# Performance work log

Hardware: AMD Instinct MI355X
Metric: run time of the kernel (lower is better)

## Reference

```python
import jax, jax.numpy as jnp
import numpy as np

N = 16384; C = 16; H = 256; W = 704
HEADS = 4; PTS = 4; K = 8; DH = C // HEADS
EPS = 1e-3  # BatchNorm eps from module

def _bn(x, g, b):
    # BatchNorm1d in training mode: batch statistics over N
    mu = x.mean(axis=0)
    var = x.var(axis=0)
    return (x - mu) * jax.lax.rsqrt(var + EPS) * g + b

def setup_inputs():
    key = jax.random.key(0)
    ks = jax.random.split(key, 20)
    def w(i, shape, s=0.25):
        return jax.random.normal(ks[i], shape, jnp.float32) * s
    grid_y = jax.random.randint(ks[0], (N,), 0, H)
    grid_x = jax.random.randint(ks[1], (N,), 0, W)
    return {
        "point_features": jax.random.normal(ks[2], (N, C), jnp.float32),
        "image_feat": jax.random.normal(ks[3], (C, H, W), jnp.float32),
        "image_grid": jnp.stack([grid_y, grid_x], axis=1),
        "Wk": w(4, (C, C)), "bk": w(5, (C,)), "gk": jnp.ones((C,)), "betak": jnp.zeros((C,)),
        "Wfc": w(6, (2, C)), "bfc": w(7, (C,)), "gfc": jnp.ones((C,)), "betafc": jnp.zeros((C,)),
        "Wt": w(8, (C, C)), "bt": w(9, (C,)), "gt": jnp.ones((C,)), "betat": jnp.zeros((C,)),
        "Woff": w(10, (C, HEADS * PTS * 2), 0.02), "boff": w(11, (HEADS * PTS * 2,), 0.5),
        "Wattn": w(12, (C, HEADS * PTS), 0.02), "battn": jnp.zeros((HEADS * PTS,)),
        "Wval": w(13, (C, C)), "bval": w(14, (C,)),
        "Wout": w(15, (C, C)), "bout": w(16, (C,)),
        "Wf": w(17, (2 * C, C)), "bf": w(18, (C,)), "gf": jnp.ones((C,)), "betaf": jnp.zeros((C,)),
    }

def _deform_attn(q, image_feat, grid_f, Woff, boff, Wattn, battn, Wval, bval, Wout, bout):
    # MSDeformAttn with 1 level: learned offsets around projected pixel, bilinear sampling
    n = q.shape[0]
    off = (q @ Woff + boff).reshape(n, HEADS, PTS, 2)
    attn = jax.nn.softmax((q @ Wattn + battn).reshape(n, HEADS, PTS), axis=-1)
    val = (image_feat.reshape(C, H * W).T @ Wval + bval).reshape(H * W, HEADS, DH)
    val_h = val.transpose(1, 0, 2)  # [HEADS, HW, DH]
    loc_y = grid_f[:, 0][:, None, None] + off[..., 0]  # [N, HEADS, PTS]
    loc_x = grid_f[:, 1][:, None, None] + off[..., 1]
    y0 = jnp.floor(loc_y); x0 = jnp.floor(loc_x)
    wy = loc_y - y0; wx = loc_x - x0

    def corner(yi, xi, wgt):
        valid = (yi >= 0) & (yi <= H - 1) & (xi >= 0) & (xi <= W - 1)
        yc = jnp.clip(yi, 0, H - 1).astype(jnp.int32)
        xc = jnp.clip(xi, 0, W - 1).astype(jnp.int32)
        idx = (yc * W + xc).transpose(1, 0, 2)  # [HEADS, N, PTS]
        g = jax.vmap(lambda v, i: v[i])(val_h, idx)  # [HEADS, N, PTS, DH]
        return g * (wgt * valid).transpose(1, 0, 2)[..., None]

    samp = (corner(y0, x0, (1 - wy) * (1 - wx))
            + corner(y0, x0 + 1, (1 - wy) * wx)
            + corner(y0 + 1, x0, wy * (1 - wx))
            + corner(y0 + 1, x0 + 1, wy * wx))  # [HEADS, N, PTS, DH]
    out = (samp * attn.transpose(1, 0, 2)[..., None]).sum(axis=2)  # [HEADS, N, DH]
    out = out.transpose(1, 0, 2).reshape(n, C)
    return out @ Wout + bout

def reference(point_features, image_feat, image_grid, Wk, bk, gk, betak, Wfc, bfc, gfc, betafc, Wt, bt, gt, betat, Woff, boff, Wattn, battn, Wval, bval, Wout, bout, Wf, bf, gf, betaf):
    grid_f = image_grid.astype(jnp.float32)
    # KNN over projected pixel coords (cKDTree.query k=K+1, drop self)
    d2 = ((grid_f[:, None, :] - grid_f[None, :, :]) ** 2).sum(-1)
    _, nidx = jax.lax.top_k(-d2, K + 1)
    nidx = nidx[:, 1:]  # [N, K]

    pts = _bn(point_features @ Wk + bk, gk, betak)  # pts_key_proj
    # normalized relative image-plane positions -> fc
    center = grid_f.mean(axis=0)
    rel = grid_f - center
    mx = jnp.abs(rel).max(axis=0)
    mx = jnp.where(mx == 0, 1.0, mx)
    pos = _bn((rel / mx) @ Wfc + bfc, gfc, betafc)

    # gather image feats at projected pixels + KNN-graph neighbor aggregation
    gathered = image_feat[:, image_grid[:, 0], image_grid[:, 1]].T  # [N, C]
    neigh = gathered[nidx].mean(axis=1)  # [N, C]

    q = pts + pos
    img_pre = _deform_attn(q, image_feat, grid_f, Woff, boff, Wattn, battn, Wval, bval, Wout, bout) + neigh

    pts_pre = _bn(pts @ Wt + bt, gt, betat)  # pts_transform
    fuse = jax.nn.relu(jnp.concatenate([pts_pre, img_pre], axis=-1))  # activate_out
    return jax.nn.relu(_bn(fuse @ Wf + bf, gf, betaf))  # fuse_conv
```

## Files before the change

### kernel.cpp

```cpp
#include <hip/hip_runtime.h>
#include <climits>

#define N_ 16384
#define H_ 256
#define W_ 704
#define HW_ (H_*W_)
#define NC_ (N_*16)
#define EPS_ 1e-3f
#define HDR_ 512

typedef unsigned long long ull;

#define VAL_   (HDR_ + 9*NC_)
#define KNNI_  (VAL_ + HW_*16)
#define PARTF_ (KNNI_ + 378256)
#define PK_    (PARTF_ + 8192)
#define PFC_   (PARTF_ + 16384)
#define PT_    (PARTF_ + 24576)

#define CAP_ 6144

__device__ __forceinline__ float wsum64(float v){
#pragma unroll
  for (int o = 32; o > 0; o >>= 1) v += __shfl_down(v, o);
  return v;
}

#define LOAD16(dst, src) { const float4* _s=(const float4*)(src); float4 _a=_s[0],_b=_s[1],_c=_s[2],_d=_s[3]; \
  dst[0]=_a.x;dst[1]=_a.y;dst[2]=_a.z;dst[3]=_a.w; dst[4]=_b.x;dst[5]=_b.y;dst[6]=_b.z;dst[7]=_b.w; \
  dst[8]=_c.x;dst[9]=_c.y;dst[10]=_c.z;dst[11]=_c.w; dst[12]=_d.x;dst[13]=_d.y;dst[14]=_d.z;dst[15]=_d.w; }

#define STORE16(dst, src) { float4* _d=(float4*)(dst); \
  _d[0]=make_float4(src[0],src[1],src[2],src[3]); _d[1]=make_float4(src[4],src[5],src[6],src[7]); \
  _d[2]=make_float4(src[8],src[9],src[10],src[11]); _d[3]=make_float4(src[12],src[13],src[14],src[15]); }

__device__ __forceinline__ void knn_insert(ull* arr, ull key){
  if (key < arr[8]){
    int q = 8;
    while (q > 0 && arr[q-1] > key){ arr[q] = arr[q-1]; --q; }
    arr[q] = key;
  }
}

__device__ __forceinline__ void scan_rows_global(const int* __restrict__ cellst,
                                                 const unsigned* __restrict__ psort,
                                                 int y, int x, int s,
                                                 int y0, int y1, int x0, int x1, ull* arr){
  for (int yy=y0+s; yy<=y1; yy+=4){
    int rowb = yy*W_;
    int st = cellst[rowb + x0];
    int e  = cellst[rowb + x1 + 1];
    int dy = y-yy, dy2 = dy*dy;
    for (int p=st; p<e; ++p){
      unsigned u = psort[p];
      int px = (int)((u>>14)&1023);
      int dx = x-px;
      knn_insert(arr, ((ull)(unsigned)(dy2+dx*dx) << 14) | (ull)(u & 16383u));
    }
  }
}

__device__ __forceinline__ void red_body(const float* __restrict__ g, const float* __restrict__ bta,
                                         const float* __restrict__ part, float* __restrict__ coef,
                                         float* __restrict__ red){
  int t = threadIdx.x, slot = t & 31, chunk = t >> 5;
  float acc = 0.f;
  for (int bb=chunk*32; bb<chunk*32+32; ++bb) acc += part[bb*32 + slot];
  red[t] = acc;
  __syncthreads();
  if (chunk == 0){
    float v = red[slot];
#pragma unroll
    for (int k2=1;k2<8;++k2) v += red[k2*32+slot];
    red[slot] = v;
  }
  __syncthreads();
  if (t < 16){
    float mu  = red[t]    * (1.f/N_);
    float var = red[16+t] * (1.f/N_) - mu*mu;
    float a = g[t] / sqrtf(var + EPS_);
    coef[t]    = a;
    coef[16+t] = bta[t] - mu*a;
  }
  __syncthreads();
}

__global__ __launch_bounds__(256) void k1(const float* __restrict__ pf,
                                          const float* __restrict__ imf,
                                          const int* __restrict__ grid,
                                          const float* __restrict__ Wk, const float* __restrict__ bk,
                                          const float* __restrict__ Wval, const float* __restrict__ bval,
                                          float* __restrict__ ws){
  __shared__ float sA[256], sB[16];
  const int t = threadIdx.x, b = blockIdx.x;
  const bool ldsK = (b >= 177 && b < 241);
  const bool ldsV = (b >= 1265);
  if (ldsK){ sA[t] = Wk[t];   if (t < 16) sB[t] = bk[t]; }
  if (ldsV){ sA[t] = Wval[t]; if (t < 16) sB[t] = bval[t]; }
  if (ldsK || ldsV) __syncthreads();

  if (b < 176){
    int4* c4 = (int4*)(ws + KNNI_);
    c4[b*256 + t] = make_int4(0,0,0,0);
  } else if (b == 176){
    if (t == 0){
      int* ih = (int*)ws;
      ih[0]=0; ih[1]=0; ih[2]=INT_MAX; ih[3]=INT_MIN; ih[4]=INT_MAX; ih[5]=INT_MIN;
      ih[6]=0; ih[7]=0;
    }
  } else if (ldsK){
    const int i = (b-177)*256 + t;
    float p[16]; LOAD16(p, pf + i*16);
    float ok[16];
#pragma unroll
    for (int c=0;c<16;++c) ok[c] = sB[c];
#pragma unroll
    for (int j=0;j<16;++j){ float v = p[j];
#pragma unroll
      for (int c=0;c<16;++c) ok[c] += v*sA[j*16+c];
    }
    STORE16(ws + HDR_ + i*16, ok);
    float* partK = ws + PK_;
    const int grp = i >> 6;
#pragma unroll
    for (int c=0;c<16;++c){
      float a = wsum64(ok[c]); float q2 = wsum64(ok[c]*ok[c]);
      if ((t&63)==0){ partK[grp*32+c]=a; partK[grp*32+16+c]=q2; }
    }
  } else if (b < 1265){
    const int idx = (b-241)*256 + t;
    const int i = idx >> 4, c = idx & 15;
    int2 g = ((const int2*)grid)[i];
    ws[HDR_ + 2*NC_ + idx] = imf[c*HW_ + g.x*W_ + g.y];
  } else {
    const int pix = (b-1265)*256 + t;
    float a[16];
#pragma unroll
    for (int ci=0;ci<16;++ci) a[ci] = imf[ci*HW_ + pix];
    float o[16];
#pragma unroll
    for (int c=0;c<16;++c) o[c] = sB[c];
#pragma unroll
    for (int ci=0;ci<16;++ci){ float v=a[ci];
#pragma unroll
      for (int c=0;c<16;++c) o[c] += v*sA[ci*16+c];
    }
    STORE16(ws + VAL_ + pix*16, o);
  }
}

__global__ __launch_bounds__(256) void k2(const int* __restrict__ grid,
                                          const float* __restrict__ gk, const float* __restrict__ betak,
                                          float* __restrict__ ws){
  const int t = threadIdx.x, b = blockIdx.x;
  if (b < 64){
    int i = b*256 + t;
    int2 p = ((const int2*)grid)[i];
    int* counts = (int*)(ws + KNNI_);
    atomicAdd(&counts[p.x*W_ + p.y], 1);
    int sy=p.x, sx=p.y, mny=p.x, mxy=p.x, mnx=p.y, mxx=p.y;
#pragma unroll
    for (int o=32;o>0;o>>=1){
      sy += __shfl_down(sy,o); sx += __shfl_down(sx,o);
      mny = min(mny,__shfl_down(mny,o)); mxy = max(mxy,__shfl_down(mxy,o));
      mnx = min(mnx,__shfl_down(mnx,o)); mxx = max(mxx,__shfl_down(mxx,o));
    }
    __shared__ int sh[24];
    int w = t >> 6;
    if ((t & 63) == 0){
      sh[w]=sy; sh[4+w]=sx; sh[8+w]=mny; sh[12+w]=mxy; sh[16+w]=mnx; sh[20+w]=mxx;
    }
    __syncthreads();
    if (t == 0){
      int a0=sh[0]+sh[1]+sh[2]+sh[3];
      int a1=sh[4]+sh[5]+sh[6]+sh[7];
      int a2=min(min(sh[8],sh[9]),min(sh[10],sh[11]));
      int a3=max(max(sh[12],sh[13]),max(sh[14],sh[15]));
      int a4=min(min(sh[16],sh[17]),min(sh[18],sh[19]));
      int a5=max(max(sh[20],sh[21]),max(sh[22],sh[23]));
      int* ih = (int*)ws;
      atomicAdd(&ih[0],a0); atomicAdd(&ih[1],a1);
      atomicMin(&ih[2],a2); atomicMax(&ih[3],a3);
      atomicMin(&ih[4],a4); atomicMax(&ih[5],a5);
    }
  } else {
    __shared__ float red[256];
    red_body(gk, betak, ws + PK_, ws + 136, red);
  }
}

__global__ __launch_bounds__(256) void k3(const float* __restrict__ Wt, const float* __restrict__ bt,
                                          float* __restrict__ ws){
  const int t = threadIdx.x, b = blockIdx.x;
  int* ih = (int*)ws;
  int* counts = (int*)(ws + KNNI_);
  int* bsum   = counts + 360464;
  int* boffp  = bsum + 704;
  if (b < 704){
    __shared__ int w4[4];
    __shared__ int sWin;
    int v = counts[b*256 + t];
#pragma unroll
    for (int o=32;o>0;o>>=1) v += __shfl_down(v,o);
    if ((t&63)==0) w4[t>>6] = v;
    __syncthreads();
    if (t == 0){
      bsum[b] = w4[0]+w4[1]+w4[2]+w4[3];
      __threadfence();
      int old = atomicAdd(&ih[6], 1);
      sWin = (old == 703) ? 1 : 0;
    }
    __syncthreads();
    if (sWin){
      if (t == 0) __threadfence();
      __syncthreads();
      if (t == 0){
        float cy = (float)ih[0] / (float)N_;
        float cx = (float)ih[1] / (float)N_;
        float my = fmaxf((float)ih[3]-cy, cy-(float)ih[2]);
        float mx = fmaxf((float)ih[5]-cx, cx-(float)ih[4]);
        if (my == 0.f) my = 1.f;
        if (mx == 0.f) mx = 1.f;
        ws[264]=cy; ws[265]=cx; ws[266]=1.f/my; ws[267]=1.f/mx;
      }
      __shared__ int sWsum[4];
      __shared__ int sCarry;
      int lane = t & 63, wv = t >> 6;
      if (t==0) sCarry = 0;
      __syncthreads();
      for (int c=0;c<3;++c){
        int idx = c*256 + t;
        int v0 = (idx < 704) ? bsum[idx] : 0;
        int vv = v0;
#pragma unroll
        for (int o=1;o<64;o<<=1){ int xx=__shfl_up(vv,o); if (lane>=o) vv+=xx; }
        if (lane==63) sWsum[wv]=vv;
        __syncthreads();
        int add = sCarry;
        for (int w2=0;w2<wv;++w2) add += sWsum[w2];
        if (idx < 704) boffp[idx] = add + vv - v0;
        __syncthreads();
        if (t==255) sCarry = add + vv;
        __syncthreads();
      }
    }
  } else {
    __shared__ float sWt[256];
    sWt[t] = Wt[t];
    __syncthreads();
    const int i = (b-704)*256 + t;
    float kA[16], kC[16];
    LOAD16(kA, ws+136); LOAD16(kC, ws+152);
    float pl[16]; LOAD16(pl, ws + HDR_ + i*16);
    float pts[16];
#pragma unroll
    for (int c=0;c<16;++c) pts[c] = pl[c]*kA[c] + kC[c];
    float tv[16];
#pragma unroll
    for (int c=0;c<16;++c) tv[c] = bt[c];
#pragma unroll
    for (int j=0;j<16;++j){ float v = pts[j];
#pragma unroll
      for (int c=0;c<16;++c) tv[c] += v*sWt[j*16+c];
    }
    STORE16(ws + HDR_ + 3*NC_ + i*16, tv);
    float* partT = ws + PT_;
    const int grp = i >> 6;
#pragma unroll
    for (int c=0;c<16;++c){
      float a = wsum64(tv[c]); float q2 = wsum64(tv[c]*tv[c]);
      if ((t&63)==0){ partT[grp*32+c]=a; partT[grp*32+16+c]=q2; }
    }
  }
}

__global__ __launch_bounds__(256) void k4(const int* __restrict__ grid,
                                          const float* __restrict__ Wfc, const float* __restrict__ bfc,
                                          const float* __restrict__ gt, const float* __restrict__ betat,
                                          float* __restrict__ ws){
  const int t = threadIdx.x, b = blockIdx.x;
  int* counts = (int*)(ws + KNNI_);
  int* cellst = counts + 180224;
  int* bsum   = counts + 360464;
  int* boffp  = bsum + 704;
  if (b < 704){
    __shared__ int sWsum[4];
    int lane = t & 63, wv = t >> 6;
    int i = b*256 + t;
    int v0 = counts[i], v = v0;
#pragma unroll
    for (int o=1;o<64;o<<=1){ int xx=__shfl_up(v,o); if (lane>=o) v+=xx; }
    if (lane==63) sWsum[wv]=v;
    __syncthreads();
    int add = boffp[b];
    for (int w2=0;w2<wv;++w2) add += sWsum[w2];
    int start = add + v - v0;
    cellst[i] = start;
    counts[i] = start;
    if (i == 0) cellst[HW_] = N_;
  } else if (b < 768){
    const int i = (b-704)*256 + t;
    float cy=ws[264], cx=ws[265], imy=ws[266], imx=ws[267];
    int2 g = ((const int2*)grid)[i];
    float ry = ((float)g.x - cy)*imy, rx = ((float)g.y - cx)*imx;
    float op[16];
#pragma unroll
    for (int c=0;c<16;++c) op[c] = ry*Wfc[c] + rx*Wfc[16+c] + bfc[c];
    STORE16(ws + HDR_ + NC_ + i*16, op);
    float* partFC = ws + PFC_;
    const int grp = i >> 6;
#pragma unroll
    for (int c=0;c<16;++c){
      float a = wsum64(op[c]); float q2 = wsum64(op[c]*op[c]);
      if ((t&63)==0){ partFC[grp*32+c]=a; partFC[grp*32+16+c]=q2; }
    }
  } else {
    __shared__ float red[256];
    red_body(gt, betat, ws + PT_, ws + 200, red);
  }
}

__global__ __launch_bounds__(256) void k5(const int* __restrict__ grid,
                                          const float* __restrict__ gfc, const float* __restrict__ betafc,
                                          float* __restrict__ ws){
  const int t = threadIdx.x, b = blockIdx.x;
  if (b < 64){
    int i = b*256 + t;
    int2 g = ((const int2*)grid)[i];
    int* counts = (int*)(ws + KNNI_);
    unsigned* psort = (unsigned*)(counts + 180224 + 180240 + 704 + 704);
    int pos = atomicAdd(&counts[g.x*W_ + g.y], 1);
    psort[pos] = ((unsigned)g.x<<24) | ((unsigned)g.y<<14) | (unsigned)i;
  } else {
    __shared__ float red[256];
    red_body(gfc, betafc, ws + PFC_, ws + 168, red);
  }
}

__global__ __launch_bounds__(256) void k6(const float* __restrict__ WoffW, const float* __restrict__ boffW,
                                          const float* __restrict__ Wattn, const float* __restrict__ battn,
                                          float* __restrict__ ws){
  const int t = threadIdx.x, b = blockIdx.x;
  if (b < 256){
    const int* cellst = (const int*)(ws + KNNI_) + 180224;
    const unsigned* psort = (const unsigned*)((const int*)(ws + KNNI_) + 180224 + 180240 + 704 + 704);
    __shared__ unsigned sBand[CAP_];
    __shared__ int sRowBase[80];
    __shared__ int sMn, sMx;
    int lane = t & 63;
    int s = t & 3, pl = t >> 2;
    int gid = b*64 + pl;
    unsigned me = psort[gid];
    int y = (int)(me>>24), x = (int)((me>>14)&1023), i = (int)(me&16383);
    if (t==0){ sMn = INT_MAX; sMx = -1; }
    __syncthreads();
    if (s==0){ atomicMin(&sMn, y); atomicMax(&sMx, y); }
    __syncthreads();
    int ya = max(sMn-16,0), yb = min(sMx+16,H_-1);
    int nr = yb-ya+1;
    int p0 = cellst[ya*W_], p1 = cellst[(yb+1)*W_];
    int count = p1-p0;
    bool fb = (count > CAP_) || (nr > 78);
    if (!fb){
      for (int j=t; j<count; j+=256) sBand[j] = psort[p0+j];
      for (int j=t; j<=nr; j+=256) sRowBase[j] = cellst[(ya+j)*W_] - p0;
    }
    __syncthreads();
    int r = 8;
    { int y0=max(y-8,0),y1=min(y+8,H_-1),x0=max(x-8,0),x1=min(x+8,W_-1);
      if ((y1-y0+1)*(x1-x0+1) < 224) r = 16; }
    ull arr[9];
#pragma unroll
    for (int q=0;q<9;++q) arr[q] = ~0ull;
    {
      int y0=max(y-r,0),y1=min(y+r,H_-1),x0=max(x-r,0),x1=min(x+r,W_-1);
      if (!fb){
        for (int yy=y0+s; yy<=y1; yy+=4){
          int j = yy-ya;
          int bb = sRowBase[j], e = sRowBase[j+1];
          int lo=bb, hi=e;
          while (lo<hi){ int mid=(lo+hi)>>1; int xm=(int)((sBand[mid]>>14)&1023); if (xm<x0) lo=mid+1; else hi=mid; }
          int dy = y-yy, dy2 = dy*dy;
          for (int p=lo; p<e; ++p){
            unsigned u = sBand[p];
            int px = (int)((u>>14)&1023);
            if (px > x1) break;
            int dx = x-px;
            knn_insert(arr, ((ull)(unsigned)(dy2+dx*dx) << 14) | (ull)(u & 16383u));
          }
        }
      } else {
        scan_rows_global(cellst, psort, y, x, s, y0, y1, x0, x1, arr);
      }
    }
    ull m[9];
    bool done = false;
    {
      ull k[9];
#pragma unroll
      for (int q=0;q<9;++q) m[q] = ~0ull;
      int base = lane & ~3;
      for (int ss=0; ss<4; ++ss){
#pragma unroll
        for (int q=0;q<9;++q) k[q] = __shfl(arr[q], base+ss);
        for (int q2=0;q2<9;++q2){
          ull kk = k[q2];
          if (kk >= m[8]) break;
          int q = 8; while (q>0 && m[q-1]>kk){ m[q]=m[q-1]; --q; } m[q]=kk;
        }
      }
      int y0=max(y-r,0),y1=min(y+r,H_-1),x0=max(x-r,0),x1=min(x+r,W_-1);
      bool covered = (y0==0)&&(y1==H_-1)&&(x0==0)&&(x1==W_-1);
      bool ok2 = covered;
      if (!ok2 && m[8] != ~0ull){ int d9 = (int)(m[8]>>14); ok2 = d9 < (r+1)*(r+1); }
      done = ok2;
    }
    while (__ballot(!done)){
      if (!done){
        r <<= 1;
        int y0=max(y-r,0),y1=min(y+r,H_-1),x0=max(x-r,0),x1=min(x+r,W_-1);
#pragma unroll
        for (int q=0;q<9;++q) arr[q] = ~0ull;
        scan_rows_global(cellst, psort, y, x, s, y0, y1, x0, x1, arr);
      }
      ull k[9];
      bool doIns = !done;
      if (doIns){
#pragma unroll
        for (int q=0;q<9;++q) m[q] = ~0ull;
      }
      int base = lane & ~3;
      for (int ss=0; ss<4; ++ss){
#pragma unroll
        for (int q=0;q<9;++q) k[q] = __shfl(arr[q], base+ss);
        if (doIns){
          for (int q2=0;q2<9;++q2){
            ull kk = k[q2];
            if (kk >= m[8]) break;
            int q = 8; while (q>0 && m[q-1]>kk){ m[q]=m[q-1]; --q; } m[q]=kk;
          }
        }
      }
      if (!done){
        int y0=max(y-r,0),y1=min(y+r,H_-1),x0=max(x-r,0),x1=min(x+r,W_-1);
        bool covered = (y0==0)&&(y1==H_-1)&&(x0==0)&&(x1==W_-1);
        bool ok2 = covered;
        if (!ok2 && m[8] != ~0ull){ int d9 = (int)(m[8]>>14); ok2 = d9 < (r+1)*(r+1); }
        if (ok2) done = true;
      }
    }
    const float* gath = ws + HDR_ + 2*NC_;
    float4 acc = make_float4(0.f,0.f,0.f,0.f);
#pragma unroll
    for (int nb=1; nb<9; ++nb){
      int idx = (int)(m[nb] & 16383ull);
      const float4 g4 = *(const float4*)(gath + idx*16 + s*4);
      acc.x += g4.x; acc.y += g4.y; acc.z += g4.z; acc.w += g4.w;
    }
    float* neigh = ws + HDR_ + 7*NC_;
    *(float4*)(neigh + i*16 + s*4) =
        make_float4(acc.x*0.125f, acc.y*0.125f, acc.z*0.125f, acc.w*0.125f);
  } else {
    __shared__ float sWoff[512], sWattn[256];
    __shared__ float sboff[32], sbattn[16];
    sWoff[t] = WoffW[t]; sWoff[256+t] = WoffW[256+t];
    sWattn[t] = Wattn[t];
    if (t < 32) sboff[t] = boffW[t];
    if (t < 16) sbattn[t] = battn[t];
    __syncthreads();
    const int i = (b-256)*256 + t;
    float kA[16],kC[16],fA[16],fC[16];
    LOAD16(kA, ws+136); LOAD16(kC, ws+152); LOAD16(fA, ws+168); LOAD16(fC, ws+184);
    float pl[16], po[16];
    LOAD16(pl, ws + HDR_ + i*16);
    LOAD16(po, ws + HDR_ + NC_ + i*16);
    float q[16];
#pragma unroll
    for (int c=0;c<16;++c) q[c] = pl[c]*kA[c]+kC[c] + po[c]*fA[c]+fC[c];
    float ov[32];
#pragma unroll
    for (int o=0;o<32;++o) ov[o] = sboff[o];
#pragma unroll
    for (int j=0;j<16;++j){ float v=q[j];
#pragma unroll
      for (int o=0;o<32;++o) ov[o] += v*sWoff[j*32+o];
    }
    { float4* d=(float4*)(ws + HDR_ + 4*NC_ + i*32);
#pragma unroll
      for (int rr=0;rr<8;++rr) d[rr]=make_float4(ov[rr*4],ov[rr*4+1],ov[rr*4+2],ov[rr*4+3]);
    }
    float l[16];
#pragma unroll
    for (int c=0;c<16;++c) l[c] = sbattn[c];
#pragma unroll
    for (int j=0;j<16;++j){ float v=q[j];
#pragma unroll
      for (int c=0;c<16;++c) l[c] += v*sWattn[j*16+c];
    }
    float av[16];
#pragma unroll
    for (int h=0;h<4;++h){
      float m = fmaxf(fmaxf(l[h*4],l[h*4+1]),fmaxf(l[h*4+2],l[h*4+3]));
      float e0=expf(l[h*4]-m), e1=expf(l[h*4+1]-m), e2=expf(l[h*4+2]-m), e3=expf(l[h*4+3]-m);
      float inv = 1.f/(e0+e1+e2+e3);
      av[h*4]=e0*inv; av[h*4+1]=e1*inv; av[h*4+2]=e2*inv; av[h*4+3]=e3*inv;
    }
    STORE16(ws + HDR_ + 6*NC_ + i*16, av);
  }
}

__global__ __launch_bounds__(256) void k7(
    const int* __restrict__ grid,
    const float* __restrict__ Wout, const float* __restrict__ bout,
    const float* __restrict__ Wf, const float* __restrict__ bf,
    const float* __restrict__ gf, const float* __restrict__ betaf,
    float* __restrict__ ws)
{
  __shared__ float sWout[256], sWf[512], sbout[16], sbf[16];
  __shared__ float sTl[1024], sNei[1024], sSamp[1024], sImg[1024];
  __shared__ float sPart[128];
  __shared__ float red[256];
  __shared__ int sWin;
  int t = threadIdx.x, b = blockIdx.x;
  int p = t >> 2, h = t & 3;
  int i = b*64 + p;
  sWout[t]=Wout[t]; sWf[t]=Wf[t]; sWf[t+256]=Wf[t+256];
  if (t<16){ sbout[t]=bout[t]; sbf[t]=bf[t]; }
  {
    const float4* tl4 = (const float4*)(ws + HDR_ + 3*NC_ + b*1024);
    const float4* nv4 = (const float4*)(ws + HDR_ + 7*NC_ + b*1024);
    float4 v = tl4[t];
    int c0 = (t*4) & 15;
    float a0=ws[200+c0],a1=ws[201+c0],a2=ws[202+c0],a3=ws[203+c0];
    float c0v=ws[216+c0],c1v=ws[217+c0],c2v=ws[218+c0],c3v=ws[219+c0];
    sTl[t*4]   = fmaxf(v.x*a0+c0v, 0.f);
    sTl[t*4+1] = fmaxf(v.y*a1+c1v, 0.f);
    sTl[t*4+2] = fmaxf(v.z*a2+c2v, 0.f);
    sTl[t*4+3] = fmaxf(v.w*a3+c3v, 0.f);
    float4 nv = nv4[t];
    sNei[t*4]=nv.x; sNei[t*4+1]=nv.y; sNei[t*4+2]=nv.z; sNei[t*4+3]=nv.w;
  }
  const float4* off4 = (const float4*)(ws + HDR_ + 4*NC_ + b*2048);
  float4 o0 = off4[t*2], o1 = off4[t*2+1];
  float4 aw = ((const float4*)(ws + HDR_ + 6*NC_ + b*1024))[t];
  int2 g = ((const int2*)grid)[i];
  float y = (float)g.x, x = (float)g.y;
  const float4* val4 = (const float4*)(ws + VAL_);
  float4 acc = make_float4(0.f,0.f,0.f,0.f);
  float offv[8] = {o0.x,o0.y,o0.z,o0.w,o1.x,o1.y,o1.z,o1.w};
  float avv[4]  = {aw.x,aw.y,aw.z,aw.w};
#define CORNER(yy,xx,wgt) do{ int _y=(yy),_x=(xx); \
    if ((unsigned)_y < (unsigned)H_ && (unsigned)_x < (unsigned)W_){ \
      float4 _v = val4[(_y*W_+_x)*4 + h]; float _w = a*(wgt); \
      acc.x += _w*_v.x; acc.y += _w*_v.y; acc.z += _w*_v.z; acc.w += _w*_v.w; } }while(0)
#pragma unroll
  for (int pt=0; pt<4; ++pt){
    float a  = avv[pt];
    float ly = y + offv[pt*2], lx = x + offv[pt*2+1];
    float fy = floorf(ly), fx = floorf(lx);
    float wy = ly - fy, wx = lx - fx;
    int y0 = (int)fy, x0 = (int)fx;
    CORNER(y0,   x0,   (1.f-wy)*(1.f-wx));
    CORNER(y0,   x0+1, (1.f-wy)*wx);
    CORNER(y0+1, x0,   wy*(1.f-wx));
    CORNER(y0+1, x0+1, wy*wx);
  }
#undef CORNER
  ((float4*)sSamp)[t] = acc;
  __syncthreads();
  float img[4];
#pragma unroll
  for (int k=0;k<4;++k){ int cc=h*4+k; img[k] = sbout[cc] + sNei[p*16+cc]; }
#pragma unroll
  for (int j=0;j<16;++j){
    float v = sSamp[p*16+j];
#pragma unroll
    for (int k=0;k<4;++k) img[k] += v*sWout[j*16 + h*4 + k];
  }
  ((float4*)sImg)[t] = make_float4(img[0],img[1],img[2],img[3]);
  __syncthreads();
  float fl[4];
#pragma unroll
  for (int k=0;k<4;++k) fl[k] = sbf[h*4+k];
#pragma unroll
  for (int j=0;j<16;++j){
    float v1 = sTl[p*16+j];
    float v2 = fmaxf(sImg[p*16+j], 0.f);
#pragma unroll
    for (int k=0;k<4;++k){
      fl[k] += v1*sWf[j*16 + h*4 + k];
      fl[k] += v2*sWf[(16+j)*16 + h*4 + k];
    }
  }
  float* f_lin = ws + HDR_ + 8*NC_;
  ((float4*)(f_lin + b*1024))[t] = make_float4(fl[0],fl[1],fl[2],fl[3]);
  float s0=fl[0],s1=fl[1],s2=fl[2],s3=fl[3];
  float q0=fl[0]*fl[0],q1=fl[1]*fl[1],q2=fl[2]*fl[2],q3=fl[3]*fl[3];
#pragma unroll
  for (int o=32;o>=4;o>>=1){
    s0+=__shfl_down(s0,o); s1+=__shfl_down(s1,o); s2+=__shfl_down(s2,o); s3+=__shfl_down(s3,o);
    q0+=__shfl_down(q0,o); q1+=__shfl_down(q1,o); q2+=__shfl_down(q2,o); q3+=__shfl_down(q3,o);
  }
  int wave = t >> 6, lane = t & 63;
  if (lane < 4){
    sPart[wave*32 + lane*4+0]=s0; sPart[wave*32 + lane*4+1]=s1;
    sPart[wave*32 + lane*4+2]=s2; sPart[wave*32 + lane*4+3]=s3;
    sPart[wave*32 + 16 + lane*4+0]=q0; sPart[wave*32 + 16 + lane*4+1]=q1;
    sPart[wave*32 + 16 + lane*4+2]=q2; sPart[wave*32 + 16 + lane*4+3]=q3;
  }
  __syncthreads();
  if (t < 32){
    float v = sPart[t]+sPart[32+t]+sPart[64+t]+sPart[96+t];
    (ws + PARTF_)[b*32 + t] = v;
  }
  __threadfence();
  __syncthreads();
  if (t == 0){
    int old = atomicAdd(&((int*)ws)[7], 1);
    sWin = (old == 255) ? 1 : 0;
  }
  __syncthreads();
  if (sWin){
    if (t == 0) __threadfence();
    __syncthreads();
    red_body(gf, betaf, ws + PARTF_, ws + 232, red);
  }
}

__global__ __launch_bounds__(256) void k8(const float* __restrict__ ws, float* __restrict__ out){
  const int gtid = blockIdx.x*256 + threadIdx.x;
  const int idx4 = gtid*4;
  float4 v = *(const float4*)(ws + HDR_ + 8*NC_ + idx4);
  const int c = idx4 & 15;
  float4 r;
  r.x = fmaxf(v.x*ws[232+c] + ws[248+c], 0.f);
  r.y = fmaxf(v.y*ws[233+c] + ws[249+c], 0.f);
  r.z = fmaxf(v.z*ws[234+c] + ws[250+c], 0.f);
  r.w = fmaxf(v.w*ws[235+c] + ws[251+c], 0.f);
  *(float4*)(out + idx4) = r;
}

extern "C" void kernel_launch(void* const* d_in, const int* in_sizes, int n_in,
                              void* d_out, int out_size, void* d_ws, size_t ws_size,
                              hipStream_t stream)
{
  (void)in_sizes; (void)n_in; (void)out_size; (void)ws_size;
  const float* pf    = (const float*)d_in[0];
  const float* imf   = (const float*)d_in[1];
  const int*   gridp = (const int*)d_in[2];
  const float* Wk   =(const float*)d_in[3],  *bk   =(const float*)d_in[4];
  const float* gk   =(const float*)d_in[5],  *betak=(const float*)d_in[6];
  const float* Wfc  =(const float*)d_in[7],  *bfc  =(const float*)d_in[8];
  const float* gfc  =(const float*)d_in[9],  *betafc=(const float*)d_in[10];
  const float* Wt   =(const float*)d_in[11], *bt   =(const float*)d_in[12];
  const float* gt   =(const float*)d_in[13], *betat=(const float*)d_in[14];
  const float* Woff =(const float*)d_in[15], *boff =(const float*)d_in[16];
  const float* Wattn=(const float*)d_in[17], *battn=(const float*)d_in[18];
  const float* Wval =(const float*)d_in[19], *bval =(const float*)d_in[20];
  const float* Wout =(const float*)d_in[21], *bout =(const float*)d_in[22];
  const float* Wf   =(const float*)d_in[23], *bf   =(const float*)d_in[24];
  const float* gf   =(const float*)d_in[25], *betaf=(const float*)d_in[26];
  float* ws  = (float*)d_ws;
  float* out = (float*)d_out;

  hipLaunchKernelGGL(k1, dim3(1969), dim3(256), 0, stream, pf, imf, gridp, Wk, bk, Wval, bval, ws);
  hipLaunchKernelGGL(k2, dim3(65),   dim3(256), 0, stream, gridp, gk, betak, ws);
  hipLaunchKernelGGL(k3, dim3(768),  dim3(256), 0, stream, Wt, bt, ws);
  hipLaunchKernelGGL(k4, dim3(769),  dim3(256), 0, stream, gridp, Wfc, bfc, gt, betat, ws);
  hipLaunchKernelGGL(k5, dim3(65),   dim3(256), 0, stream, gridp, gfc, betafc, ws);
  hipLaunchKernelGGL(k6, dim3(320),  dim3(256), 0, stream, Woff, boff, Wattn, battn, ws);
  hipLaunchKernelGGL(k7, dim3(256),  dim3(256), 0, stream, gridp, Wout, bout, Wf, bf, gf, betaf, ws);
  hipLaunchKernelGGL(k8, dim3(256),  dim3(256), 0, stream, ws, out);
}
```

Measured before the change: 230.8 us.

## Replace counting-sort KNN grid with fixed-slot cell buckets and merge kernels

Replaces the prefix-sum/counting-sort spatial grid for KNN with per-pixel fixed 8-slot buckets filled by atomics, so the scan and scatter kernels disappear. The KNN search now walks every cell in the box, checks its count and reads the slots. Batch-norm coefficient reductions are recomputed redundantly in each consuming block instead of through last-block election and atomics. Eight launches become five. Walking every cell in the box adds reads for sparse regions, and cells holding more than 8 points silently drop the extras.

```diff
diff --git a/kernel.cpp b/kernel.cpp
--- a/kernel.cpp
+++ b/kernel.cpp
@@ -11,14 +11,13 @@
 
 typedef unsigned long long ull;
 
-#define VAL_   (HDR_ + 9*NC_)
-#define KNNI_  (VAL_ + HW_*16)
-#define PARTF_ (KNNI_ + 378256)
-#define PK_    (PARTF_ + 8192)
-#define PFC_   (PARTF_ + 16384)
-#define PT_    (PARTF_ + 24576)
-
-#define CAP_ 6144
+#define VAL_    (HDR_ + 9*NC_)
+#define KNNI_   (VAL_ + HW_*16)
+#define PARTK_  (KNNI_ + 1622016)
+#define PARTFC_ (PARTK_ + 8192)
+#define PARTT_  (PARTK_ + 16384)
+#define PARTF2_ (PARTK_ + 24576)
+#define SPI_    (PARTK_ + 32768)
 
 __device__ __forceinline__ float wsum64(float v){
 #pragma unroll
@@ -42,20 +41,24 @@
   }
 }
 
-__device__ __forceinline__ void scan_rows_global(const int* __restrict__ cellst,
-                                                 const unsigned* __restrict__ psort,
-                                                 int y, int x, int s,
-                                                 int y0, int y1, int x0, int x1, ull* arr){
+__device__ __forceinline__ void scan_box_padded(const int* __restrict__ counts,
+                                                const unsigned* __restrict__ slots,
+                                                int y, int x, int s,
+                                                int y0, int y1, int x0, int x1, ull* arr){
   for (int yy=y0+s; yy<=y1; yy+=4){
     int rowb = yy*W_;
-    int st = cellst[rowb + x0];
-    int e  = cellst[rowb + x1 + 1];
     int dy = y-yy, dy2 = dy*dy;
-    for (int p=st; p<e; ++p){
-      unsigned u = psort[p];
-      int px = (int)((u>>14)&1023);
-      int dx = x-px;
-      knn_insert(arr, ((ull)(unsigned)(dy2+dx*dx) << 14) | (ull)(u & 16383u));
+    for (int xx=x0; xx<=x1; ++xx){
+      int c = counts[rowb+xx];
+      if (c){
+        c = min(c, 8);
+        const unsigned* sl = slots + (ull)(rowb+xx)*8;
+        int dx = x-xx, d2 = dy2 + dx*dx;
+        for (int k=0;k<c;++k){
+          unsigned u = sl[k];
+          knn_insert(arr, ((ull)(unsigned)d2 << 14) | (ull)(u & 16383u));
+        }
+      }
     }
   }
 }
@@ -85,31 +88,66 @@
   __syncthreads();
 }
 
+__global__ __launch_bounds__(256) void k0(const int* __restrict__ grid, float* __restrict__ ws){
+  const int t = threadIdx.x, b = blockIdx.x;
+  if (b < 176){
+    int4* c4 = (int4*)(ws + KNNI_);
+    c4[b*256 + t] = make_int4(0,0,0,0);
+  } else {
+    const int sb = b - 176;
+    int2 p = ((const int2*)grid)[sb*256 + t];
+    int sy=p.x, sx=p.y, mny=p.x, mxy=p.x, mnx=p.y, mxx=p.y;
+#pragma unroll
+    for (int o=32;o>0;o>>=1){
+      sy += __shfl_down(sy,o); sx += __shfl_down(sx,o);
+      mny = min(mny,__shfl_down(mny,o)); mxy = max(mxy,__shfl_down(mxy,o));
+      mnx = min(mnx,__shfl_down(mnx,o)); mxx = max(mxx,__shfl_down(mxx,o));
+    }
+    __shared__ int sh[24];
+    int w = t >> 6;
+    if ((t & 63) == 0){
+      sh[w]=sy; sh[4+w]=sx; sh[8+w]=mny; sh[12+w]=mxy; sh[16+w]=mnx; sh[20+w]=mxx;
+    }
+    __syncthreads();
+    if (t == 0){
+      int* sp = (int*)ws + SPI_ + sb*8;
+      sp[0]=sh[0]+sh[1]+sh[2]+sh[3];
+      sp[1]=sh[4]+sh[5]+sh[6]+sh[7];
+      sp[2]=min(min(sh[8],sh[9]),min(sh[10],sh[11]));
+      sp[3]=max(max(sh[12],sh[13]),max(sh[14],sh[15]));
+      sp[4]=min(min(sh[16],sh[17]),min(sh[18],sh[19]));
+      sp[5]=max(max(sh[20],sh[21]),max(sh[22],sh[23]));
+    }
+  }
+}
+
 __global__ __launch_bounds__(256) void k1(const float* __restrict__ pf,
                                           const float* __restrict__ imf,
                                           const int* __restrict__ grid,
                                           const float* __restrict__ Wk, const float* __restrict__ bk,
+                                          const float* __restrict__ Wfc, const float* __restrict__ bfc,
                                           const float* __restrict__ Wval, const float* __restrict__ bval,
                                           float* __restrict__ ws){
   __shared__ float sA[256], sB[16];
+  __shared__ float sctr[4];
   const int t = threadIdx.x, b = blockIdx.x;
-  const bool ldsK = (b >= 177 && b < 241);
-  const bool ldsV = (b >= 1265);
+  const bool ldsK = (b >= 64 && b < 128);
+  const bool ldsV = (b >= 1216);
   if (ldsK){ sA[t] = Wk[t];   if (t < 16) sB[t] = bk[t]; }
   if (ldsV){ sA[t] = Wval[t]; if (t < 16) sB[t] = bval[t]; }
   if (ldsK || ldsV) __syncthreads();
 
-  if (b < 176){
-    int4* c4 = (int4*)(ws + KNNI_);
-    c4[b*256 + t] = make_int4(0,0,0,0);
-  } else if (b == 176){
-    if (t == 0){
-      int* ih = (int*)ws;
-      ih[0]=0; ih[1]=0; ih[2]=INT_MAX; ih[3]=INT_MIN; ih[4]=INT_MAX; ih[5]=INT_MIN;
-      ih[6]=0; ih[7]=0;
-    }
+  if (b < 64){
+    const int i = b*256 + t;
+    int2 g = ((const int2*)grid)[i];
+    int* counts = (int*)(ws + KNNI_);
+    unsigned* slots = (unsigned*)(counts + 180224);
+    int cell = g.x*W_ + g.y;
+    int pos = atomicAdd(&counts[cell], 1);
+    if (pos < 8)
+      slots[(ull)cell*8 + pos] = ((unsigned)g.x<<24) | ((unsigned)g.y<<14) | (unsigned)i;
   } else if (ldsK){
-    const int i = (b-177)*256 + t;
+    const int i = (b-64)*256 + t;
     float p[16]; LOAD16(p, pf + i*16);
     float ok[16];
 #pragma unroll
@@ -120,20 +158,54 @@
       for (int c=0;c<16;++c) ok[c] += v*sA[j*16+c];
     }
     STORE16(ws + HDR_ + i*16, ok);
-    float* partK = ws + PK_;
+    float* partK = ws + PARTK_;
     const int grp = i >> 6;
 #pragma unroll
     for (int c=0;c<16;++c){
       float a = wsum64(ok[c]); float q2 = wsum64(ok[c]*ok[c]);
       if ((t&63)==0){ partK[grp*32+c]=a; partK[grp*32+16+c]=q2; }
     }
-  } else if (b < 1265){
-    const int idx = (b-241)*256 + t;
+  } else if (b < 192){
+    if (t < 64){
+      const int* sp = (const int*)ws + SPI_ + t*8;
+      int sy=sp[0], sx=sp[1], mny=sp[2], mxy=sp[3], mnx=sp[4], mxx=sp[5];
+#pragma unroll
+      for (int o=32;o>0;o>>=1){
+        sy += __shfl_down(sy,o); sx += __shfl_down(sx,o);
+        mny = min(mny,__shfl_down(mny,o)); mxy = max(mxy,__shfl_down(mxy,o));
+        mnx = min(mnx,__shfl_down(mnx,o)); mxx = max(mxx,__shfl_down(mxx,o));
+      }
+      if (t == 0){
+        float cy = (float)sy / (float)N_;
+        float cx = (float)sx / (float)N_;
+        float my = fmaxf((float)mxy-cy, cy-(float)mny); if (my==0.f) my=1.f;
+        float mx = fmaxf((float)mxx-cx, cx-(float)mnx); if (mx==0.f) mx=1.f;
+        sctr[0]=cy; sctr[1]=cx; sctr[2]=1.f/my; sctr[3]=1.f/mx;
+      }
+    }
+    __syncthreads();
+    const int i = (b-128)*256 + t;
+    float cy=sctr[0], cx=sctr[1], imy=sctr[2], imx=sctr[3];
+    int2 g = ((const int2*)grid)[i];
+    float ry = ((float)g.x - cy)*imy, rx = ((float)g.y - cx)*imx;
+    float op[16];
+#pragma unroll
+    for (int c=0;c<16;++c) op[c] = ry*Wfc[c] + rx*Wfc[16+c] + bfc[c];
+    STORE16(ws + HDR_ + NC_ + i*16, op);
+    float* partFC = ws + PARTFC_;
+    const int grp = i >> 6;
+#pragma unroll
+    for (int c=0;c<16;++c){
+      float a = wsum64(op[c]); float q2 = wsum64(op[c]*op[c]);
+      if ((t&63)==0){ partFC[grp*32+c]=a; partFC[grp*32+16+c]=q2; }
+    }
+  } else if (b < 1216){
+    const int idx = (b-192)*256 + t;
     const int i = idx >> 4, c = idx & 15;
     int2 g = ((const int2*)grid)[i];
     ws[HDR_ + 2*NC_ + idx] = imf[c*HW_ + g.x*W_ + g.y];
   } else {
-    const int pix = (b-1265)*256 + t;
+    const int pix = (b-1216)*256 + t;
     float a[16];
 #pragma unroll
     for (int ci=0;ci<16;++ci) a[ci] = imf[ci*HW_ + pix];
@@ -150,222 +222,23 @@
 }
 
 __global__ __launch_bounds__(256) void k2(const int* __restrict__ grid,
+                                          const float* __restrict__ Wt, const float* __restrict__ bt,
                                           const float* __restrict__ gk, const float* __restrict__ betak,
-                                          float* __restrict__ ws){
-  const int t = threadIdx.x, b = blockIdx.x;
-  if (b < 64){
-    int i = b*256 + t;
-    int2 p = ((const int2*)grid)[i];
-    int* counts = (int*)(ws + KNNI_);
-    atomicAdd(&counts[p.x*W_ + p.y], 1);
-    int sy=p.x, sx=p.y, mny=p.x, mxy=p.x, mnx=p.y, mxx=p.y;
-#pragma unroll
-    for (int o=32;o>0;o>>=1){
-      sy += __shfl_down(sy,o); sx += __shfl_down(sx,o);
-      mny = min(mny,__shfl_down(mny,o)); mxy = max(mxy,__shfl_down(mxy,o));
-      mnx = min(mnx,__shfl_down(mnx,o)); mxx = max(mxx,__shfl_down(mxx,o));
-    }
-    __shared__ int sh[24];
-    int w = t >> 6;
-    if ((t & 63) == 0){
-      sh[w]=sy; sh[4+w]=sx; sh[8+w]=mny; sh[12+w]=mxy; sh[16+w]=mnx; sh[20+w]=mxx;
-    }
-    __syncthreads();
-    if (t == 0){
-      int a0=sh[0]+sh[1]+sh[2]+sh[3];
-      int a1=sh[4]+sh[5]+sh[6]+sh[7];
-      int a2=min(min(sh[8],sh[9]),min(sh[10],sh[11]));
-      int a3=max(max(sh[12],sh[13]),max(sh[14],sh[15]));
-      int a4=min(min(sh[16],sh[17]),min(sh[18],sh[19]));
-      int a5=max(max(sh[20],sh[21]),max(sh[22],sh[23]));
-      int* ih = (int*)ws;
-      atomicAdd(&ih[0],a0); atomicAdd(&ih[1],a1);
-      atomicMin(&ih[2],a2); atomicMax(&ih[3],a3);
-      atomicMin(&ih[4],a4); atomicMax(&ih[5],a5);
-    }
-  } else {
-    __shared__ float red[256];
-    red_body(gk, betak, ws + PK_, ws + 136, red);
-  }
-}
-
-__global__ __launch_bounds__(256) void k3(const float* __restrict__ Wt, const float* __restrict__ bt,
-                                          float* __restrict__ ws){
-  const int t = threadIdx.x, b = blockIdx.x;
-  int* ih = (int*)ws;
-  int* counts = (int*)(ws + KNNI_);
-  int* bsum   = counts + 360464;
-  int* boffp  = bsum + 704;
-  if (b < 704){
-    __shared__ int w4[4];
-    __shared__ int sWin;
-    int v = counts[b*256 + t];
-#pragma unroll
-    for (int o=32;o>0;o>>=1) v += __shfl_down(v,o);
-    if ((t&63)==0) w4[t>>6] = v;
-    __syncthreads();
-    if (t == 0){
-      bsum[b] = w4[0]+w4[1]+w4[2]+w4[3];
-      __threadfence();
-      int old = atomicAdd(&ih[6], 1);
-      sWin = (old == 703) ? 1 : 0;
-    }
-    __syncthreads();
-    if (sWin){
-      if (t == 0) __threadfence();
-      __syncthreads();
-      if (t == 0){
-        float cy = (float)ih[0] / (float)N_;
-        float cx = (float)ih[1] / (float)N_;
-        float my = fmaxf((float)ih[3]-cy, cy-(float)ih[2]);
-        float mx = fmaxf((float)ih[5]-cx, cx-(float)ih[4]);
-        if (my == 0.f) my = 1.f;
-        if (mx == 0.f) mx = 1.f;
-        ws[264]=cy; ws[265]=cx; ws[266]=1.f/my; ws[267]=1.f/mx;
-      }
-      __shared__ int sWsum[4];
-      __shared__ int sCarry;
-      int lane = t & 63, wv = t >> 6;
-      if (t==0) sCarry = 0;
-      __syncthreads();
-      for (int c=0;c<3;++c){
-        int idx = c*256 + t;
-        int v0 = (idx < 704) ? bsum[idx] : 0;
-        int vv = v0;
-#pragma unroll
-        for (int o=1;o<64;o<<=1){ int xx=__shfl_up(vv,o); if (lane>=o) vv+=xx; }
-        if (lane==63) sWsum[wv]=vv;
-        __syncthreads();
-        int add = sCarry;
-        for (int w2=0;w2<wv;++w2) add += sWsum[w2];
-        if (idx < 704) boffp[idx] = add + vv - v0;
-        __syncthreads();
-        if (t==255) sCarry = add + vv;
-        __syncthreads();
-      }
-    }
-  } else {
-    __shared__ float sWt[256];
-    sWt[t] = Wt[t];
-    __syncthreads();
-    const int i = (b-704)*256 + t;
-    float kA[16], kC[16];
-    LOAD16(kA, ws+136); LOAD16(kC, ws+152);
-    float pl[16]; LOAD16(pl, ws + HDR_ + i*16);
-    float pts[16];
-#pragma unroll
-    for (int c=0;c<16;++c) pts[c] = pl[c]*kA[c] + kC[c];
-    float tv[16];
-#pragma unroll
-    for (int c=0;c<16;++c) tv[c] = bt[c];
-#pragma unroll
-    for (int j=0;j<16;++j){ float v = pts[j];
-#pragma unroll
-      for (int c=0;c<16;++c) tv[c] += v*sWt[j*16+c];
-    }
-    STORE16(ws + HDR_ + 3*NC_ + i*16, tv);
-    float* partT = ws + PT_;
-    const int grp = i >> 6;
-#pragma unroll
-    for (int c=0;c<16;++c){
-      float a = wsum64(tv[c]); float q2 = wsum64(tv[c]*tv[c]);
-      if ((t&63)==0){ partT[grp*32+c]=a; partT[grp*32+16+c]=q2; }
-    }
-  }
-}
-
-__global__ __launch_bounds__(256) void k4(const int* __restrict__ grid,
-                                          const float* __restrict__ Wfc, const float* __restrict__ bfc,
-                                          const float* __restrict__ gt, const float* __restrict__ betat,
-                                          float* __restrict__ ws){
-  const int t = threadIdx.x, b = blockIdx.x;
-  int* counts = (int*)(ws + KNNI_);
-  int* cellst = counts + 180224;
-  int* bsum   = counts + 360464;
-  int* boffp  = bsum + 704;
-  if (b < 704){
-    __shared__ int sWsum[4];
-    int lane = t & 63, wv = t >> 6;
-    int i = b*256 + t;
-    int v0 = counts[i], v = v0;
-#pragma unroll
-    for (int o=1;o<64;o<<=1){ int xx=__shfl_up(v,o); if (lane>=o) v+=xx; }
-    if (lane==63) sWsum[wv]=v;
-    __syncthreads();
-    int add = boffp[b];
-    for (int w2=0;w2<wv;++w2) add += sWsum[w2];
-    int start = add + v - v0;
-    cellst[i] = start;
-    counts[i] = start;
-    if (i == 0) cellst[HW_] = N_;
-  } else if (b < 768){
-    const int i = (b-704)*256 + t;
-    float cy=ws[264], cx=ws[265], imy=ws[266], imx=ws[267];
-    int2 g = ((const int2*)grid)[i];
-    float ry = ((float)g.x - cy)*imy, rx = ((float)g.y - cx)*imx;
-    float op[16];
-#pragma unroll
-    for (int c=0;c<16;++c) op[c] = ry*Wfc[c] + rx*Wfc[16+c] + bfc[c];
-    STORE16(ws + HDR_ + NC_ + i*16, op);
-    float* partFC = ws + PFC_;
-    const int grp = i >> 6;
-#pragma unroll
-    for (int c=0;c<16;++c){
-      float a = wsum64(op[c]); float q2 = wsum64(op[c]*op[c]);
-      if ((t&63)==0){ partFC[grp*32+c]=a; partFC[grp*32+16+c]=q2; }
-    }
-  } else {
-    __shared__ float red[256];
-    red_body(gt, betat, ws + PT_, ws + 200, red);
-  }
-}
-
-__global__ __launch_bounds__(256) void k5(const int* __restrict__ grid,
                                           const float* __restrict__ gfc, const float* __restrict__ betafc,
-                                          float* __restrict__ ws){
-  const int t = threadIdx.x, b = blockIdx.x;
-  if (b < 64){
-    int i = b*256 + t;
-    int2 g = ((const int2*)grid)[i];
-    int* counts = (int*)(ws + KNNI_);
-    unsigned* psort = (unsigned*)(counts + 180224 + 180240 + 704 + 704);
-    int pos = atomicAdd(&counts[g.x*W_ + g.y], 1);
-    psort[pos] = ((unsigned)g.x<<24) | ((unsigned)g.y<<14) | (unsigned)i;
-  } else {
-    __shared__ float red[256];
-    red_body(gfc, betafc, ws + PFC_, ws + 168, red);
-  }
-}
-
-__global__ __launch_bounds__(256) void k6(const float* __restrict__ WoffW, const float* __restrict__ boffW,
+                                          const float* __restrict__ WoffW, const float* __restrict__ boffW,
                                           const float* __restrict__ Wattn, const float* __restrict__ battn,
                                           float* __restrict__ ws){
   const int t = threadIdx.x, b = blockIdx.x;
+  __shared__ float sWt[256], sWoff[512], sWattn[256], sboff[32], sbattn[16];
+  __shared__ float red[256], coefA[32], coefB[32];
   if (b < 256){
-    const int* cellst = (const int*)(ws + KNNI_) + 180224;
-    const unsigned* psort = (const unsigned*)((const int*)(ws + KNNI_) + 180224 + 180240 + 704 + 704);
-    __shared__ unsigned sBand[CAP_];
-    __shared__ int sRowBase[80];
-    __shared__ int sMn, sMx;
-    int lane = t & 63;
-    int s = t & 3, pl = t >> 2;
-    int gid = b*64 + pl;
-    unsigned me = psort[gid];
-    int y = (int)(me>>24), x = (int)((me>>14)&1023), i = (int)(me&16383);
-    if (t==0){ sMn = INT_MAX; sMx = -1; }
-    __syncthreads();
-    if (s==0){ atomicMin(&sMn, y); atomicMax(&sMx, y); }
-    __syncthreads();
-    int ya = max(sMn-16,0), yb = min(sMx+16,H_-1);
-    int nr = yb-ya+1;
-    int p0 = cellst[ya*W_], p1 = cellst[(yb+1)*W_];
-    int count = p1-p0;
-    bool fb = (count > CAP_) || (nr > 78);
-    if (!fb){
-      for (int j=t; j<count; j+=256) sBand[j] = psort[p0+j];
-      for (int j=t; j<=nr; j+=256) sRowBase[j] = cellst[(ya+j)*W_] - p0;
-    }
-    __syncthreads();
+    const int* counts = (const int*)(ws + KNNI_);
+    const unsigned* slots = (const unsigned*)(counts + 180224);
+    const int lane = t & 63;
+    const int s = t & 3, pl = t >> 2;
+    const int i = b*64 + pl;
+    int2 g = ((const int2*)grid)[i];
+    int y = g.x, x = g.y;
     int r = 8;
     { int y0=max(y-8,0),y1=min(y+8,H_-1),x0=max(x-8,0),x1=min(x+8,W_-1);
       if ((y1-y0+1)*(x1-x0+1) < 224) r = 16; }
@@ -374,24 +247,7 @@
     for (int q=0;q<9;++q) arr[q] = ~0ull;
     {
       int y0=max(y-r,0),y1=min(y+r,H_-1),x0=max(x-r,0),x1=min(x+r,W_-1);
-      if (!fb){
-        for (int yy=y0+s; yy<=y1; yy+=4){
-          int j = yy-ya;
-          int bb = sRowBase[j], e = sRowBase[j+1];
-          int lo=bb, hi=e;
-          while (lo<hi){ int mid=(lo+hi)>>1; int xm=(int)((sBand[mid]>>14)&1023); if (xm<x0) lo=mid+1; else hi=mid; }
-          int dy = y-yy, dy2 = dy*dy;
-          for (int p=lo; p<e; ++p){
-            unsigned u = sBand[p];
-            int px = (int)((u>>14)&1023);
-            if (px > x1) break;
-            int dx = x-px;
-            knn_insert(arr, ((ull)(unsigned)(dy2+dx*dx) << 14) | (ull)(u & 16383u));
-          }
-        }
-      } else {
-        scan_rows_global(cellst, psort, y, x, s, y0, y1, x0, x1, arr);
-      }
+      scan_box_padded(counts, slots, y, x, s, y0, y1, x0, x1, arr);
     }
     ull m[9];
     bool done = false;
@@ -421,7 +277,7 @@
         int y0=max(y-r,0),y1=min(y+r,H_-1),x0=max(x-r,0),x1=min(x+r,W_-1);
 #pragma unroll
         for (int q=0;q<9;++q) arr[q] = ~0ull;
-        scan_rows_global(cellst, psort, y, x, s, y0, y1, x0, x1, arr);
+        scan_box_padded(counts, slots, y, x, s, y0, y1, x0, x1, arr);
       }
       ull k[9];
       bool doIns = !done;
@@ -444,7 +300,7 @@
       if (!done){
         int y0=max(y-r,0),y1=min(y+r,H_-1),x0=max(x-r,0),x1=min(x+r,W_-1);
         bool covered = (y0==0)&&(y1==H_-1)&&(x0==0)&&(x1==W_-1);
-        bool ok2 = covered;
+        bool ok2 = covered || (r > 1024);
         if (!ok2 && m[8] != ~0ull){ int d9 = (int)(m[8]>>14); ok2 = d9 < (r+1)*(r+1); }
         if (ok2) done = true;
       }
@@ -460,23 +316,47 @@
     float* neigh = ws + HDR_ + 7*NC_;
     *(float4*)(neigh + i*16 + s*4) =
         make_float4(acc.x*0.125f, acc.y*0.125f, acc.z*0.125f, acc.w*0.125f);
+  } else if (b < 320){
+    sWt[t] = Wt[t];
+    __syncthreads();
+    red_body(gk, betak, ws + PARTK_, coefA, red);
+    const int i = (b-256)*256 + t;
+    float pl[16]; LOAD16(pl, ws + HDR_ + i*16);
+    float pts[16];
+#pragma unroll
+    for (int c=0;c<16;++c) pts[c] = pl[c]*coefA[c] + coefA[16+c];
+    float tv[16];
+#pragma unroll
+    for (int c=0;c<16;++c) tv[c] = bt[c];
+#pragma unroll
+    for (int j=0;j<16;++j){ float v = pts[j];
+#pragma unroll
+      for (int c=0;c<16;++c) tv[c] += v*sWt[j*16+c];
+    }
+    STORE16(ws + HDR_ + 3*NC_ + i*16, tv);
+    float* partT = ws + PARTT_;
+    const int grp = i >> 6;
+#pragma unroll
+    for (int c=0;c<16;++c){
+      float a = wsum64(tv[c]); float q2 = wsum64(tv[c]*tv[c]);
+      if ((t&63)==0){ partT[grp*32+c]=a; partT[grp*32+16+c]=q2; }
+    }
   } else {
-    __shared__ float sWoff[512], sWattn[256];
-    __shared__ float sboff[32], sbattn[16];
     sWoff[t] = WoffW[t]; sWoff[256+t] = WoffW[256+t];
     sWattn[t] = Wattn[t];
     if (t < 32) sboff[t] = boffW[t];
     if (t < 16) sbattn[t] = battn[t];
     __syncthreads();
-    const int i = (b-256)*256 + t;
-    float kA[16],kC[16],fA[16],fC[16];
-    LOAD16(kA, ws+136); LOAD16(kC, ws+152); LOAD16(fA, ws+168); LOAD16(fC, ws+184);
+    red_body(gk, betak, ws + PARTK_, coefA, red);
+    red_body(gfc, betafc, ws + PARTFC_, coefB, red);
+    const int i = (b-320)*256 + t;
     float pl[16], po[16];
     LOAD16(pl, ws + HDR_ + i*16);
     LOAD16(po, ws + HDR_ + NC_ + i*16);
     float q[16];
 #pragma unroll
-    for (int c=0;c<16;++c) q[c] = pl[c]*kA[c]+kC[c] + po[c]*fA[c]+fC[c];
+    for (int c=0;c<16;++c)
+      q[c] = pl[c]*coefA[c]+coefA[16+c] + po[c]*coefB[c]+coefB[16+c];
     float ov[32];
 #pragma unroll
     for (int o=0;o<32;++o) ov[o] = sboff[o];
@@ -509,30 +389,30 @@
   }
 }
 
-__global__ __launch_bounds__(256) void k7(
+__global__ __launch_bounds__(256) void k3(
     const int* __restrict__ grid,
     const float* __restrict__ Wout, const float* __restrict__ bout,
     const float* __restrict__ Wf, const float* __restrict__ bf,
-    const float* __restrict__ gf, const float* __restrict__ betaf,
+    const float* __restrict__ gt, const float* __restrict__ betat,
     float* __restrict__ ws)
 {
   __shared__ float sWout[256], sWf[512], sbout[16], sbf[16];
   __shared__ float sTl[1024], sNei[1024], sSamp[1024], sImg[1024];
   __shared__ float sPart[128];
-  __shared__ float red[256];
-  __shared__ int sWin;
+  __shared__ float red[256], coefT[32];
   int t = threadIdx.x, b = blockIdx.x;
   int p = t >> 2, h = t & 3;
   int i = b*64 + p;
   sWout[t]=Wout[t]; sWf[t]=Wf[t]; sWf[t+256]=Wf[t+256];
   if (t<16){ sbout[t]=bout[t]; sbf[t]=bf[t]; }
+  red_body(gt, betat, ws + PARTT_, coefT, red);
   {
     const float4* tl4 = (const float4*)(ws + HDR_ + 3*NC_ + b*1024);
     const float4* nv4 = (const float4*)(ws + HDR_ + 7*NC_ + b*1024);
     float4 v = tl4[t];
     int c0 = (t*4) & 15;
-    float a0=ws[200+c0],a1=ws[201+c0],a2=ws[202+c0],a3=ws[203+c0];
-    float c0v=ws[216+c0],c1v=ws[217+c0],c2v=ws[218+c0],c3v=ws[219+c0];
+    float a0=coefT[c0],a1=coefT[c0+1],a2=coefT[c0+2],a3=coefT[c0+3];
+    float c0v=coefT[16+c0],c1v=coefT[17+c0],c2v=coefT[18+c0],c3v=coefT[19+c0];
     sTl[t*4]   = fmaxf(v.x*a0+c0v, 0.f);
     sTl[t*4+1] = fmaxf(v.y*a1+c1v, 0.f);
     sTl[t*4+2] = fmaxf(v.z*a2+c2v, 0.f);
@@ -611,32 +491,23 @@
   __syncthreads();
   if (t < 32){
     float v = sPart[t]+sPart[32+t]+sPart[64+t]+sPart[96+t];
-    (ws + PARTF_)[b*32 + t] = v;
-  }
-  __threadfence();
-  __syncthreads();
-  if (t == 0){
-    int old = atomicAdd(&((int*)ws)[7], 1);
-    sWin = (old == 255) ? 1 : 0;
-  }
-  __syncthreads();
-  if (sWin){
-    if (t == 0) __threadfence();
-    __syncthreads();
-    red_body(gf, betaf, ws + PARTF_, ws + 232, red);
-  }
-}
-
-__global__ __launch_bounds__(256) void k8(const float* __restrict__ ws, float* __restrict__ out){
+    (ws + PARTF2_)[b*32 + t] = v;
+  }
+}
+
+__global__ __launch_bounds__(256) void k4(const float* __restrict__ gf, const float* __restrict__ betaf,
+                                          float* __restrict__ ws, float* __restrict__ out){
+  __shared__ float red[256], coefF[32];
+  red_body(gf, betaf, ws + PARTF2_, coefF, red);
   const int gtid = blockIdx.x*256 + threadIdx.x;
   const int idx4 = gtid*4;
   float4 v = *(const float4*)(ws + HDR_ + 8*NC_ + idx4);
   const int c = idx4 & 15;
   float4 r;
-  r.x = fmaxf(v.x*ws[232+c] + ws[248+c], 0.f);
-  r.y = fmaxf(v.y*ws[233+c] + ws[249+c], 0.f);
-  r.z = fmaxf(v.z*ws[234+c] + ws[250+c], 0.f);
-  r.w = fmaxf(v.w*ws[235+c] + ws[251+c], 0.f);
+  r.x = fmaxf(v.x*coefF[c]   + coefF[16+c],   0.f);
+  r.y = fmaxf(v.y*coefF[c+1] + coefF[17+c],   0.f);
+  r.z = fmaxf(v.z*coefF[c+2] + coefF[18+c],   0.f);
+  r.w = fmaxf(v.w*coefF[c+3] + coefF[19+c],   0.f);
   *(float4*)(out + idx4) = r;
 }
 
@@ -663,12 +534,9 @@
   float* ws  = (float*)d_ws;
   float* out = (float*)d_out;
 
-  hipLaunchKernelGGL(k1, dim3(1969), dim3(256), 0, stream, pf, imf, gridp, Wk, bk, Wval, bval, ws);
-  hipLaunchKernelGGL(k2, dim3(65),   dim3(256), 0, stream, gridp, gk, betak, ws);
-  hipLaunchKernelGGL(k3, dim3(768),  dim3(256), 0, stream, Wt, bt, ws);
-  hipLaunchKernelGGL(k4, dim3(769),  dim3(256), 0, stream, gridp, Wfc, bfc, gt, betat, ws);
-  hipLaunchKernelGGL(k5, dim3(65),   dim3(256), 0, stream, gridp, gfc, betafc, ws);
-  hipLaunchKernelGGL(k6, dim3(320),  dim3(256), 0, stream, Woff, boff, Wattn, battn, ws);
-  hipLaunchKernelGGL(k7, dim3(256),  dim3(256), 0, stream, gridp, Wout, bout, Wf, bf, gf, betaf, ws);
-  hipLaunchKernelGGL(k8, dim3(256),  dim3(256), 0, stream, ws, out);
-}
+  hipLaunchKernelGGL(k0, dim3(240),  dim3(256), 0, stream, gridp, ws);
+  hipLaunchKernelGGL(k1, dim3(1920), dim3(256), 0, stream, pf, imf, gridp, Wk, bk, Wfc, bfc, Wval, bval, ws);
+  hipLaunchKernelGGL(k2, dim3(384),  dim3(256), 0, stream, gridp, Wt, bt, gk, betak, gfc, betafc, Woff, boff, Wattn, battn, ws);
+  hipLaunchKernelGGL(k3, dim3(256),  dim3(256), 0, stream, gridp, Wout, bout, Wf, bf, gt, betat, ws);
+  hipLaunchKernelGGL(k4, dim3(256),  dim3(256), 0, stream, gf, betaf, ws, out);
+}
```

Result: slower. 284.3 us (+23.2%).
